# Performance work log

Hardware: AMD Instinct MI355X
Metric: run time of the kernel (lower is better)

Reference implementation:

```python
import jax, jax.numpy as jnp
import numpy as np

EPS = 0.97  # ContrastLoss eps
T = 0.07    # temperature

def _embed(x, W, b):
    # Linear + L2 normalize (Normalize(power=2))
    h = x @ W.T + b                     # [B, feat_dim]
    norm = jnp.sqrt(jnp.sum(h * h, axis=1, keepdims=True))
    return h / norm

def setup_inputs() -> dict:
    key = jax.random.key(0)
    ks = jax.random.split(key, 7)
    B, S, Td, F = 8192, 2048, 2048, 128
    return {
        "f_s": jax.random.normal(ks[0], (B, S), jnp.float32),
        "f_t": jax.random.normal(ks[1], (B, Td), jnp.float32),
        "y": jax.random.randint(ks[2], (B,), 0, 100, jnp.int64),
        "W_s": jax.random.normal(ks[3], (F, S), jnp.float32) * 0.02,
        "b_s": jax.random.normal(ks[4], (F,), jnp.float32) * 0.02,
        "W_t": jax.random.normal(ks[5], (F, Td), jnp.float32) * 0.02,
        "b_t": jax.random.normal(ks[6], (F,), jnp.float32) * 0.02,
    }

def reference(f_s, f_t, y, W_s, b_s, W_t, b_t):
    fs = _embed(f_s, W_s, b_s)
    ft = _embed(f_t, W_t, b_t)
    # CRDLoss re-normalizes (idempotent, kept for fidelity)
    fs = fs / jnp.linalg.norm(fs, axis=1, keepdims=True)
    ft = ft / jnp.linalg.norm(ft, axis=1, keepdims=True)
    bsz = fs.shape[0]
    x = jnp.exp((fs @ ft.T) / T)  # [B, B] exponentiated similarities
    same = y[None, :] == y[:, None]        # y_expand == y_expand.T
    diag = jnp.eye(bsz, dtype=bool)
    pos_mask = same & ~diag
    neg_mask = ~same & ~diag
    # masked log-ratio sums instead of dynamic-shape gathers
    log_D1 = jnp.log(x / (x + EPS))
    log_D0 = jnp.log(EPS / (x + EPS))
    loss = -(jnp.sum(jnp.where(pos_mask, log_D1, 0.0))
             + jnp.sum(jnp.where(neg_mask, log_D0, 0.0))) / bsz
    return loss
```

## Files before the change

### kernel.cpp

```cpp
#include <hip/hip_runtime.h>
#include <math.h>


typedef _Float16 half_t;
typedef half_t halfx4 __attribute__((ext_vector_type(4)));
typedef half_t halfx8 __attribute__((ext_vector_type(8)));
typedef float f32x4 __attribute__((ext_vector_type(4)));

#define B_TOT   8192
#define K_EMB   2048
#define F_DIM   128
#define INV_T   14.285714285714286f
#define EPS_C   0.97f
#define LOG_EPS (-0.030459207485f)

__global__ __launch_bounds__(256) void cvt_w_kernel(
    const float* __restrict__ Ws, const float* __restrict__ Wt,
    half_t* __restrict__ Ws16, half_t* __restrict__ Wt16)
{
    const float* src = blockIdx.y ? Wt : Ws;
    half_t* dst = blockIdx.y ? Wt16 : Ws16;
    int pos4 = blockIdx.x * 256 + threadIdx.x;
    float4 v = *(const float4*)(src + (size_t)pos4 * 4);
    halfx4 h4 = {(half_t)v.x, (half_t)v.y, (half_t)v.z, (half_t)v.w};
    *(halfx4*)(dst + (size_t)pos4 * 4) = h4;
}

__global__ __launch_bounds__(256) void embed_kernel(
    const float* __restrict__ Xs, const float* __restrict__ Xt,
    const half_t* __restrict__ Ws16, const half_t* __restrict__ Wt16,
    const float* __restrict__ bs, const float* __restrict__ bt,
    half_t* __restrict__ outs, half_t* __restrict__ outt)
{
    const float* X; const half_t* W16; const float* bias; half_t* out;
    if (blockIdx.y == 0) { X = Xs; W16 = Ws16; bias = bs; out = outs; }
    else                 { X = Xt; W16 = Wt16; bias = bt; out = outt; }

    __shared__ uint4 As4[2][16 * 16];
    __shared__ uint4 Bs4[2][128 * 16];
    __shared__ float biasS[128];
    __shared__ float redS[16][4];
    __shared__ float invS[16];

    const int tid = threadIdx.x;
    const int r0  = blockIdx.x * 16;
    if (tid < 128) biasS[tid] = bias[tid];

    const int lane = tid & 63;
    const int w    = tid >> 6;
    const int l16  = lane & 15, lhi = lane >> 4;

    const int ph = (blockIdx.x & 1) * 8;

    f32x4 acc[2];
    acc[0] = f32x4{0.f, 0.f, 0.f, 0.f};
    acc[1] = f32x4{0.f, 0.f, 0.f, 0.f};

    const int arow = tid >> 4, ac = tid & 15;

    float4 na0, na1; uint4 nb[8];

    {
        const int kb = ph * 128;
        na0 = *(const float4*)(X + (size_t)(r0 + arow) * K_EMB + kb + ac * 8);
        na1 = *(const float4*)(X + (size_t)(r0 + arow) * K_EMB + kb + ac * 8 + 4);
#pragma unroll
        for (int i = 0; i < 8; ++i) {
            int g = tid + i * 256;
            nb[i] = *(const uint4*)(W16 + (size_t)(g >> 4) * K_EMB + kb + (g & 15) * 8);
        }
        halfx8 h8 = {(half_t)na0.x, (half_t)na0.y, (half_t)na0.z, (half_t)na0.w,
                     (half_t)na1.x, (half_t)na1.y, (half_t)na1.z, (half_t)na1.w};
        *(halfx8*)&As4[0][arow * 16 + (ac ^ arow)] = h8;
#pragma unroll
        for (int i = 0; i < 8; ++i) {
            int g = tid + i * 256;
            Bs4[0][(g >> 4) * 16 + ((g & 15) ^ ((g >> 4) & 15))] = nb[i];
        }
    }
    __syncthreads();

    for (int it = 0; it < 16; ++it) {
        const int cur = it & 1;
        if (it < 15) {
            const int kb = (((it + 1 + ph) & 15)) * 128;
            na0 = *(const float4*)(X + (size_t)(r0 + arow) * K_EMB + kb + ac * 8);
            na1 = *(const float4*)(X + (size_t)(r0 + arow) * K_EMB + kb + ac * 8 + 4);
#pragma unroll
            for (int i = 0; i < 8; ++i) {
                int g = tid + i * 256;
                nb[i] = *(const uint4*)(W16 + (size_t)(g >> 4) * K_EMB + kb + (g & 15) * 8);
            }
        }
#pragma unroll
        for (int kk = 0; kk < 4; ++kk) {
            halfx8 a, b[2];
            a = *(const halfx8*)&As4[cur][l16 * 16 + ((kk * 4 + lhi) ^ l16)];
#pragma unroll
            for (int in = 0; in < 2; ++in) {
                int r = w * 32 + in * 16 + l16;
                b[in] = *(const halfx8*)&Bs4[cur][r * 16 + ((kk * 4 + lhi) ^ l16)];
            }
#pragma unroll
            for (int in = 0; in < 2; ++in)
                acc[in] = __builtin_amdgcn_mfma_f32_16x16x32_f16(a, b[in], acc[in], 0, 0, 0);
        }
        if (it < 15) {
            const int nxt = cur ^ 1;
            halfx8 h8 = {(half_t)na0.x, (half_t)na0.y, (half_t)na0.z, (half_t)na0.w,
                         (half_t)na1.x, (half_t)na1.y, (half_t)na1.z, (half_t)na1.w};
            *(halfx8*)&As4[nxt][arow * 16 + (ac ^ arow)] = h8;
#pragma unroll
            for (int i = 0; i < 8; ++i) {
                int g = tid + i * 256;
                Bs4[nxt][(g >> 4) * 16 + ((g & 15) ^ ((g >> 4) & 15))] = nb[i];
            }
        }
        __syncthreads();
    }

    float h[2][4];
    float psum[4];
#pragma unroll
    for (int reg = 0; reg < 4; ++reg) {
        float p = 0.f;
#pragma unroll
        for (int in = 0; in < 2; ++in) {
            int col = w * 32 + in * 16 + l16;
            float v = acc[in][reg] + biasS[col];
            h[in][reg] = v;
            p += v * v;
        }
        p += __shfl_xor(p, 1);
        p += __shfl_xor(p, 2);
        p += __shfl_xor(p, 4);
        p += __shfl_xor(p, 8);
        psum[reg] = p;
    }
    if (l16 == 0)
#pragma unroll
        for (int reg = 0; reg < 4; ++reg)
            redS[lhi * 4 + reg][w] = psum[reg];
    __syncthreads();
    if (tid < 16)
        invS[tid] = rsqrtf(redS[tid][0] + redS[tid][1] + redS[tid][2] + redS[tid][3]);
    __syncthreads();

#pragma unroll
    for (int in = 0; in < 2; ++in)
#pragma unroll
        for (int reg = 0; reg < 4; ++reg) {
            int row = lhi * 4 + reg;
            int col = w * 32 + in * 16 + l16;
            out[(size_t)(r0 + row) * F_DIM + col] = (half_t)(h[in][reg] * invS[row]);
        }
}

__global__ __launch_bounds__(256) void loss_kernel(
    const half_t* __restrict__ FS, const half_t* __restrict__ FT,
    const int* __restrict__ y, double* __restrict__ partials)
{
    __shared__ uint4 As4[128 * 8];
    __shared__ uint4 Bs4[128 * 8];
    __shared__ int   yrl[128], ycl[128];
    __shared__ float wsum[4];

    const int tid = threadIdx.x;
    const int i0  = blockIdx.x * 128;
    const int j0  = blockIdx.y * 128;

    if (tid < 128) yrl[tid] = y[i0 + tid];
    else           ycl[tid - 128] = y[j0 + tid - 128];

    const int lane = tid & 63;
    const int w    = tid >> 6;
    const int wm   = w >> 1, wn = w & 1;
    const int l16  = lane & 15, lhi = lane >> 4;

#pragma unroll
    for (int i = 0; i < 4; ++i) {
        int f = tid + i * 256;
        int row = f >> 3, c = f & 7;
        As4[row * 8 + (c ^ (row & 7))] = *(const uint4*)(FS + (size_t)(i0 + row) * F_DIM + c * 8);
    }
#pragma unroll
    for (int i = 0; i < 4; ++i) {
        int f = tid + i * 256;
        int row = f >> 3, c = f & 7;
        Bs4[row * 8 + (c ^ (row & 7))] = *(const uint4*)(FT + (size_t)(j0 + row) * F_DIM + c * 8);
    }
    __syncthreads();

    f32x4 acc[4][4];
    for (int im = 0; im < 4; ++im)
        for (int in = 0; in < 4; ++in)
            acc[im][in] = f32x4{0.f, 0.f, 0.f, 0.f};

    for (int kc = 0; kc < 2; ++kc) {
#pragma unroll
        for (int kk = 0; kk < 2; ++kk) {
            halfx8 a[4], b[4];
#pragma unroll
            for (int im = 0; im < 4; ++im) {
                int r = wm * 64 + im * 16 + l16;
                a[im] = *(const halfx8*)&As4[r * 8 + ((kk * 4 + lhi) ^ (r & 7))];
            }
#pragma unroll
            for (int in = 0; in < 4; ++in) {
                int r = wn * 64 + in * 16 + l16;
                b[in] = *(const halfx8*)&Bs4[r * 8 + ((kk * 4 + lhi) ^ (r & 7))];
            }
#pragma unroll
            for (int im = 0; im < 4; ++im)
#pragma unroll
                for (int in = 0; in < 4; ++in)
                    acc[im][in] = __builtin_amdgcn_mfma_f32_16x16x32_f16(
                        a[im], b[in], acc[im][in], 0, 0, 0);
        }
        if (kc == 0) {
            __syncthreads();
#pragma unroll
            for (int i = 0; i < 4; ++i) {
                int f = tid + i * 256;
                int row = f >> 3, c = f & 7;
                As4[row * 8 + (c ^ (row & 7))] =
                    *(const uint4*)(FS + (size_t)(i0 + row) * F_DIM + 64 + c * 8);
            }
#pragma unroll
            for (int i = 0; i < 4; ++i) {
                int f = tid + i * 256;
                int row = f >> 3, c = f & 7;
                Bs4[row * 8 + (c ^ (row & 7))] =
                    *(const uint4*)(FT + (size_t)(j0 + row) * F_DIM + 64 + c * 8);
            }
            __syncthreads();
        }
    }

    float local = 0.f;
    for (int im = 0; im < 4; ++im) {
        for (int reg = 0; reg < 4; ++reg) {
            int il = wm * 64 + im * 16 + lhi * 4 + reg;
            int yi = yrl[il];
            int gi = i0 + il;
            for (int in = 0; in < 4; ++in) {
                int jl = wn * 64 + in * 16 + l16;
                float s  = acc[im][in][reg];
                float sT = s * INV_T;
                float e  = __expf(sT);
                float l  = __logf(e + EPS_C);
                float term = (yi == ycl[jl]) ? (sT - l) : (LOG_EPS - l);
                if (gi != (j0 + jl)) local += term;
            }
        }
    }
    for (int m = 1; m < 64; m <<= 1) local += __shfl_xor(local, m);
    if (lane == 0) wsum[w] = local;
    __syncthreads();
    if (tid == 0)
        partials[blockIdx.y * gridDim.x + blockIdx.x] =
            ((double)wsum[0] + (double)wsum[1]) + ((double)wsum[2] + (double)wsum[3]);
}

__global__ __launch_bounds__(256) void finalize_kernel(
    const double* __restrict__ partials, float* __restrict__ out)
{
    __shared__ double sh[4];
    double loc = 0.0;
    for (int i = threadIdx.x; i < 4096; i += 256) loc += partials[i];
    for (int m = 1; m < 64; m <<= 1) loc += __shfl_xor(loc, m);
    int lane = threadIdx.x & 63, w = threadIdx.x >> 6;
    if (lane == 0) sh[w] = loc;
    __syncthreads();
    if (threadIdx.x == 0)
        out[0] = (float)(-(sh[0] + sh[1] + sh[2] + sh[3]) / (double)B_TOT);
}

extern "C" void kernel_launch(void* const* d_in, const int* in_sizes, int n_in,
                              void* d_out, int out_size, void* d_ws, size_t ws_size,
                              hipStream_t stream)
{
    const size_t WS_NEEDED = (64 << 10) + (4 << 20) + (1 << 20);
    if (ws_size < WS_NEEDED) return;

    const float* f_s = (const float*)d_in[0];
    const float* f_t = (const float*)d_in[1];
    const int*   y   = (const int*)d_in[2];
    const float* W_s = (const float*)d_in[3];
    const float* b_s = (const float*)d_in[4];
    const float* W_t = (const float*)d_in[5];
    const float* b_t = (const float*)d_in[6];
    float* out = (float*)d_out;

    char* ws = (char*)d_ws;
    double* partials = (double*)ws;
    half_t* fs   = (half_t*)(ws + (64 << 10));
    half_t* ft   = (half_t*)(ws + (64 << 10) + (2 << 20));
    half_t* Ws16 = (half_t*)(ws + (64 << 10) + (4 << 20));
    half_t* Wt16 = (half_t*)(ws + (64 << 10) + (4 << 20) + (512 << 10));

    cvt_w_kernel<<<dim3(256, 2), 256, 0, stream>>>(W_s, W_t, Ws16, Wt16);
    embed_kernel<<<dim3(512, 2), 256, 0, stream>>>(f_s, f_t, Ws16, Wt16, b_s, b_t, fs, ft);
    loss_kernel<<<dim3(64, 64), 256, 0, stream>>>(fs, ft, y, partials);
    finalize_kernel<<<1, 256, 0, stream>>>(partials, out);
    (void)in_sizes; (void)n_in; (void)out_size;
}
```

Before: 223.5 us.

## Load A fragments directly from global into registers, shrink K tile to 64

The embed GEMM kernel stops staging the activation tile in shared memory. Each lane now loads its own MFMA A fragment from global memory and converts it to fp16 in registers. The K tile drops from 128 to 64, which doubles the iteration count but halves the shared-memory W buffer and the register prefetch footprint. The per-block phase offset that staggered K start positions is removed, which may raise channel contention on the W reads, and the per-lane A loads are less coalesced.

```diff
diff --git a/kernel.cpp b/kernel.cpp
--- a/kernel.cpp
+++ b/kernel.cpp
@@ -36,8 +36,7 @@
     if (blockIdx.y == 0) { X = Xs; W16 = Ws16; bias = bs; out = outs; }
     else                 { X = Xt; W16 = Wt16; bias = bt; out = outt; }
 
-    __shared__ uint4 As4[2][16 * 16];
-    __shared__ uint4 Bs4[2][128 * 16];
+    __shared__ uint4 Bs4[2][128 * 8];
     __shared__ float biasS[128];
     __shared__ float redS[16][4];
     __shared__ float invS[16];
@@ -50,71 +49,64 @@
     const int w    = tid >> 6;
     const int l16  = lane & 15, lhi = lane >> 4;
 
-    const int ph = (blockIdx.x & 1) * 8;
+    const float* Arow = X + (size_t)(r0 + l16) * K_EMB + lhi * 8;
+
+    const int brow = tid >> 3;
+    const int bc   = tid & 7;
 
     f32x4 acc[2];
     acc[0] = f32x4{0.f, 0.f, 0.f, 0.f};
     acc[1] = f32x4{0.f, 0.f, 0.f, 0.f};
 
-    const int arow = tid >> 4, ac = tid & 15;
-
-    float4 na0, na1; uint4 nb[8];
-
-    {
-        const int kb = ph * 128;
-        na0 = *(const float4*)(X + (size_t)(r0 + arow) * K_EMB + kb + ac * 8);
-        na1 = *(const float4*)(X + (size_t)(r0 + arow) * K_EMB + kb + ac * 8 + 4);
-#pragma unroll
-        for (int i = 0; i < 8; ++i) {
-            int g = tid + i * 256;
-            nb[i] = *(const uint4*)(W16 + (size_t)(g >> 4) * K_EMB + kb + (g & 15) * 8);
-        }
-        halfx8 h8 = {(half_t)na0.x, (half_t)na0.y, (half_t)na0.z, (half_t)na0.w,
-                     (half_t)na1.x, (half_t)na1.y, (half_t)na1.z, (half_t)na1.w};
-        *(halfx8*)&As4[0][arow * 16 + (ac ^ arow)] = h8;
-#pragma unroll
-        for (int i = 0; i < 8; ++i) {
-            int g = tid + i * 256;
-            Bs4[0][(g >> 4) * 16 + ((g & 15) ^ ((g >> 4) & 15))] = nb[i];
-        }
-    }
-    __syncthreads();
-
-    for (int it = 0; it < 16; ++it) {
+    float4 a0[2], a1[2];
+    float4 p0[2], p1[2];
+    uint4  nb[4];
+
+    a0[0] = *(const float4*)(Arow);
+    a1[0] = *(const float4*)(Arow + 4);
+    a0[1] = *(const float4*)(Arow + 32);
+    a1[1] = *(const float4*)(Arow + 36);
+#pragma unroll
+    for (int i = 0; i < 4; ++i) {
+        int row = brow + i * 32;
+        Bs4[0][row * 8 + (bc ^ (row & 7))] =
+            *(const uint4*)(W16 + (size_t)row * K_EMB + bc * 8);
+    }
+    __syncthreads();
+
+    for (int it = 0; it < 32; ++it) {
         const int cur = it & 1;
-        if (it < 15) {
-            const int kb = (((it + 1 + ph) & 15)) * 128;
-            na0 = *(const float4*)(X + (size_t)(r0 + arow) * K_EMB + kb + ac * 8);
-            na1 = *(const float4*)(X + (size_t)(r0 + arow) * K_EMB + kb + ac * 8 + 4);
-#pragma unroll
-            for (int i = 0; i < 8; ++i) {
-                int g = tid + i * 256;
-                nb[i] = *(const uint4*)(W16 + (size_t)(g >> 4) * K_EMB + kb + (g & 15) * 8);
-            }
-        }
-#pragma unroll
-        for (int kk = 0; kk < 4; ++kk) {
-            halfx8 a, b[2];
-            a = *(const halfx8*)&As4[cur][l16 * 16 + ((kk * 4 + lhi) ^ l16)];
+        if (it < 31) {
+            const int kn = (it + 1) * 64;
+            p0[0] = *(const float4*)(Arow + kn);
+            p1[0] = *(const float4*)(Arow + kn + 4);
+            p0[1] = *(const float4*)(Arow + kn + 32);
+            p1[1] = *(const float4*)(Arow + kn + 36);
+#pragma unroll
+            for (int i = 0; i < 4; ++i) {
+                int row = brow + i * 32;
+                nb[i] = *(const uint4*)(W16 + (size_t)row * K_EMB + kn + bc * 8);
+            }
+        }
+#pragma unroll
+        for (int kk = 0; kk < 2; ++kk) {
+            halfx8 a = {(half_t)a0[kk].x, (half_t)a0[kk].y, (half_t)a0[kk].z, (half_t)a0[kk].w,
+                        (half_t)a1[kk].x, (half_t)a1[kk].y, (half_t)a1[kk].z, (half_t)a1[kk].w};
 #pragma unroll
             for (int in = 0; in < 2; ++in) {
-                int r = w * 32 + in * 16 + l16;
-                b[in] = *(const halfx8*)&Bs4[cur][r * 16 + ((kk * 4 + lhi) ^ l16)];
-            }
-#pragma unroll
-            for (int in = 0; in < 2; ++in)
-                acc[in] = __builtin_amdgcn_mfma_f32_16x16x32_f16(a, b[in], acc[in], 0, 0, 0);
-        }
-        if (it < 15) {
+                int row = w * 32 + in * 16 + l16;
+                halfx8 b = *(const halfx8*)&Bs4[cur][row * 8 + ((kk * 4 + lhi) ^ (l16 & 7))];
+                acc[in] = __builtin_amdgcn_mfma_f32_16x16x32_f16(a, b, acc[in], 0, 0, 0);
+            }
+        }
+        if (it < 31) {
             const int nxt = cur ^ 1;
-            halfx8 h8 = {(half_t)na0.x, (half_t)na0.y, (half_t)na0.z, (half_t)na0.w,
-                         (half_t)na1.x, (half_t)na1.y, (half_t)na1.z, (half_t)na1.w};
-            *(halfx8*)&As4[nxt][arow * 16 + (ac ^ arow)] = h8;
-#pragma unroll
-            for (int i = 0; i < 8; ++i) {
-                int g = tid + i * 256;
-                Bs4[nxt][(g >> 4) * 16 + ((g & 15) ^ ((g >> 4) & 15))] = nb[i];
-            }
+#pragma unroll
+            for (int i = 0; i < 4; ++i) {
+                int row = brow + i * 32;
+                Bs4[nxt][row * 8 + (bc ^ (row & 7))] = nb[i];
+            }
+            a0[0] = p0[0]; a1[0] = p1[0]; a0[1] = p0[1]; a1[1] = p1[1];
         }
         __syncthreads();
     }
```

Result: slower. 256.4 us (+14.7%).

## Restructure embed GEMM to hold W fragments in registers and widen row tile

Applied to the files above, without the earlier changes.

Each embed block now processes 32 rows instead of 16. Each wave keeps a 512-wide K slice of its W columns in registers, reused across two 16-row chunks. Only the activation tile goes through double-buffered LDS, and partial sums are accumulated in an LDS fp32 tile that is bias-added and normalized at the end. This halves redundant W reads per row and removes the W LDS staging. The cost is heavy register use (32 halfx8 fragments per thread), extra LDS read-modify-write accumulation traffic, and fewer blocks.

```diff
diff --git a/kernel.cpp b/kernel.cpp
--- a/kernel.cpp
+++ b/kernel.cpp
@@ -36,124 +36,112 @@
     if (blockIdx.y == 0) { X = Xs; W16 = Ws16; bias = bs; out = outs; }
     else                 { X = Xt; W16 = Wt16; bias = bt; out = outt; }
 
-    __shared__ uint4 As4[2][16 * 16];
-    __shared__ uint4 Bs4[2][128 * 16];
+    __shared__ uint4 Abuf[2][16 * 64];
+    __shared__ float accS[32][132];
     __shared__ float biasS[128];
-    __shared__ float redS[16][4];
-    __shared__ float invS[16];
 
     const int tid = threadIdx.x;
-    const int r0  = blockIdx.x * 16;
+    const int r0  = blockIdx.x * 32;
+
+    for (int i = tid; i < 32 * 132; i += 256) ((float*)accS)[i] = 0.f;
     if (tid < 128) biasS[tid] = bias[tid];
 
     const int lane = tid & 63;
     const int w    = tid >> 6;
     const int l16  = lane & 15, lhi = lane >> 4;
 
-    const int ph = (blockIdx.x & 1) * 8;
-
-    f32x4 acc[2];
-    acc[0] = f32x4{0.f, 0.f, 0.f, 0.f};
-    acc[1] = f32x4{0.f, 0.f, 0.f, 0.f};
-
-    const int arow = tid >> 4, ac = tid & 15;
-
-    float4 na0, na1; uint4 nb[8];
+    float4 av[8];
+    halfx8 Wf[2][16];
 
     {
-        const int kb = ph * 128;
-        na0 = *(const float4*)(X + (size_t)(r0 + arow) * K_EMB + kb + ac * 8);
-        na1 = *(const float4*)(X + (size_t)(r0 + arow) * K_EMB + kb + ac * 8 + 4);
+        const float* base = X + (size_t)r0 * K_EMB;
 #pragma unroll
         for (int i = 0; i < 8; ++i) {
-            int g = tid + i * 256;
-            nb[i] = *(const uint4*)(W16 + (size_t)(g >> 4) * K_EMB + kb + (g & 15) * 8);
-        }
-        halfx8 h8 = {(half_t)na0.x, (half_t)na0.y, (half_t)na0.z, (half_t)na0.w,
-                     (half_t)na1.x, (half_t)na1.y, (half_t)na1.z, (half_t)na1.w};
-        *(halfx8*)&As4[0][arow * 16 + (ac ^ arow)] = h8;
+            int f = tid + i * 256;
+            av[i] = *(const float4*)(base + (size_t)(f >> 7) * K_EMB + (f & 127) * 4);
+        }
 #pragma unroll
         for (int i = 0; i < 8; ++i) {
-            int g = tid + i * 256;
-            Bs4[0][(g >> 4) * 16 + ((g & 15) ^ ((g >> 4) & 15))] = nb[i];
-        }
-    }
-    __syncthreads();
-
-    for (int it = 0; it < 16; ++it) {
-        const int cur = it & 1;
-        if (it < 15) {
-            const int kb = (((it + 1 + ph) & 15)) * 128;
-            na0 = *(const float4*)(X + (size_t)(r0 + arow) * K_EMB + kb + ac * 8);
-            na1 = *(const float4*)(X + (size_t)(r0 + arow) * K_EMB + kb + ac * 8 + 4);
-#pragma unroll
-            for (int i = 0; i < 8; ++i) {
-                int g = tid + i * 256;
-                nb[i] = *(const uint4*)(W16 + (size_t)(g >> 4) * K_EMB + kb + (g & 15) * 8);
-            }
-        }
-#pragma unroll
-        for (int kk = 0; kk < 4; ++kk) {
-            halfx8 a, b[2];
-            a = *(const halfx8*)&As4[cur][l16 * 16 + ((kk * 4 + lhi) ^ l16)];
-#pragma unroll
-            for (int in = 0; in < 2; ++in) {
-                int r = w * 32 + in * 16 + l16;
-                b[in] = *(const halfx8*)&Bs4[cur][r * 16 + ((kk * 4 + lhi) ^ l16)];
-            }
-#pragma unroll
-            for (int in = 0; in < 2; ++in)
-                acc[in] = __builtin_amdgcn_mfma_f32_16x16x32_f16(a, b[in], acc[in], 0, 0, 0);
-        }
-        if (it < 15) {
-            const int nxt = cur ^ 1;
-            halfx8 h8 = {(half_t)na0.x, (half_t)na0.y, (half_t)na0.z, (half_t)na0.w,
-                         (half_t)na1.x, (half_t)na1.y, (half_t)na1.z, (half_t)na1.w};
-            *(halfx8*)&As4[nxt][arow * 16 + (ac ^ arow)] = h8;
-#pragma unroll
-            for (int i = 0; i < 8; ++i) {
-                int g = tid + i * 256;
-                Bs4[nxt][(g >> 4) * 16 + ((g & 15) ^ ((g >> 4) & 15))] = nb[i];
-            }
-        }
-        __syncthreads();
-    }
-
-    float h[2][4];
-    float psum[4];
-#pragma unroll
-    for (int reg = 0; reg < 4; ++reg) {
-        float p = 0.f;
-#pragma unroll
-        for (int in = 0; in < 2; ++in) {
-            int col = w * 32 + in * 16 + l16;
-            float v = acc[in][reg] + biasS[col];
-            h[in][reg] = v;
-            p += v * v;
-        }
-        p += __shfl_xor(p, 1);
-        p += __shfl_xor(p, 2);
-        p += __shfl_xor(p, 4);
-        p += __shfl_xor(p, 8);
-        psum[reg] = p;
-    }
-    if (l16 == 0)
-#pragma unroll
-        for (int reg = 0; reg < 4; ++reg)
-            redS[lhi * 4 + reg][w] = psum[reg];
-    __syncthreads();
-    if (tid < 16)
-        invS[tid] = rsqrtf(redS[tid][0] + redS[tid][1] + redS[tid][2] + redS[tid][3]);
-    __syncthreads();
-
-#pragma unroll
-    for (int in = 0; in < 2; ++in)
-#pragma unroll
-        for (int reg = 0; reg < 4; ++reg) {
-            int row = lhi * 4 + reg;
-            int col = w * 32 + in * 16 + l16;
-            out[(size_t)(r0 + row) * F_DIM + col] = (half_t)(h[in][reg] * invS[row]);
-        }
+            int f = tid + i * 256;
+            int row = f >> 7, c = f & 127;
+            int phys = row * 64 + ((c >> 1) ^ row);
+            halfx4 h = {(half_t)av[i].x, (half_t)av[i].y, (half_t)av[i].z, (half_t)av[i].w};
+            *(halfx4*)((half_t*)&Abuf[0][phys] + (c & 1) * 4) = h;
+        }
+    }
+    __syncthreads();
+
+    for (int ks = 0; ks < 4; ++ks) {
+#pragma unroll
+        for (int g = 0; g < 2; ++g)
+#pragma unroll
+            for (int j = 0; j < 16; ++j)
+                Wf[g][j] = *(const halfx8*)(W16 +
+                    (size_t)((w * 2 + g) * 16 + l16) * K_EMB + ks * 512 + j * 32 + lhi * 8);
+
+#pragma unroll
+        for (int rc = 0; rc < 2; ++rc) {
+            const int it  = ks * 2 + rc;
+            const int cur = it & 1;
+            if (it < 7) {
+                const int ksn = (it + 1) >> 1, rcn = (it + 1) & 1;
+                const float* base = X + (size_t)(r0 + rcn * 16) * K_EMB + ksn * 512;
+#pragma unroll
+                for (int i = 0; i < 8; ++i) {
+                    int f = tid + i * 256;
+                    av[i] = *(const float4*)(base + (size_t)(f >> 7) * K_EMB + (f & 127) * 4);
+                }
+            }
+            f32x4 acc0 = f32x4{0.f, 0.f, 0.f, 0.f};
+            f32x4 acc1 = f32x4{0.f, 0.f, 0.f, 0.f};
+#pragma unroll
+            for (int j = 0; j < 16; ++j) {
+                halfx8 a = *(const halfx8*)&Abuf[cur][l16 * 64 + ((j * 4 + lhi) ^ l16)];
+                acc0 = __builtin_amdgcn_mfma_f32_16x16x32_f16(a, Wf[0][j], acc0, 0, 0, 0);
+                acc1 = __builtin_amdgcn_mfma_f32_16x16x32_f16(a, Wf[1][j], acc1, 0, 0, 0);
+            }
+#pragma unroll
+            for (int reg = 0; reg < 4; ++reg) {
+                int m = rc * 16 + lhi * 4 + reg;
+                accS[m][(w * 2 + 0) * 16 + l16] += acc0[reg];
+                accS[m][(w * 2 + 1) * 16 + l16] += acc1[reg];
+            }
+            if (it < 7) {
+                const int nxt = cur ^ 1;
+#pragma unroll
+                for (int i = 0; i < 8; ++i) {
+                    int f = tid + i * 256;
+                    int row = f >> 7, c = f & 127;
+                    int phys = row * 64 + ((c >> 1) ^ row);
+                    halfx4 h = {(half_t)av[i].x, (half_t)av[i].y, (half_t)av[i].z, (half_t)av[i].w};
+                    *(halfx4*)((half_t*)&Abuf[nxt][phys] + (c & 1) * 4) = h;
+                }
+            }
+            __syncthreads();
+        }
+    }
+
+    {
+        const int r = tid >> 3, oct = tid & 7;
+        float vals[16];
+        float s = 0.f;
+#pragma unroll
+        for (int q = 0; q < 16; ++q) {
+            float v = accS[r][oct * 16 + q] + biasS[oct * 16 + q];
+            vals[q] = v;
+            s += v * v;
+        }
+        s += __shfl_xor(s, 1);
+        s += __shfl_xor(s, 2);
+        s += __shfl_xor(s, 4);
+        const float inv = rsqrtf(s);
+        halfx8 o0, o1;
+#pragma unroll
+        for (int q = 0; q < 8; ++q) { o0[q] = (half_t)(vals[q] * inv); o1[q] = (half_t)(vals[q + 8] * inv); }
+        half_t* dst = out + (size_t)(r0 + r) * F_DIM + oct * 16;
+        *(halfx8*)dst = o0;
+        *(halfx8*)(dst + 8) = o1;
+    }
 }
 
 __global__ __launch_bounds__(256) void loss_kernel(
@@ -300,7 +288,7 @@
     half_t* Wt16 = (half_t*)(ws + (64 << 10) + (4 << 20) + (512 << 10));
 
     cvt_w_kernel<<<dim3(256, 2), 256, 0, stream>>>(W_s, W_t, Ws16, Wt16);
-    embed_kernel<<<dim3(512, 2), 256, 0, stream>>>(f_s, f_t, Ws16, Wt16, b_s, b_t, fs, ft);
+    embed_kernel<<<dim3(256, 2), 256, 0, stream>>>(f_s, f_t, Ws16, Wt16, b_s, b_t, fs, ft);
     loss_kernel<<<dim3(64, 64), 256, 0, stream>>>(fs, ft, y, partials);
     finalize_kernel<<<1, 256, 0, stream>>>(partials, out);
     (void)in_sizes; (void)n_in; (void)out_size;
```

New measurement: 235.0 us. 1.05x slower.
